# Kernel optimization log

Measured on AMD Instinct MI355X. Metric: run time of the kernel, lower is better.

## Reference

```python
import jax, jax.numpy as jnp
import numpy as np

L2_REG = 0.25

def setup_inputs() -> dict:
    key = jax.random.key(0)
    k0, k1, k2, k3 = jax.random.split(key, 4)
    B, D, A, K = 16384, 128, 8192, 64
    image_embed = jax.random.normal(k0, (B, D), dtype=jnp.float32)
    anc_ind = jax.random.randint(k1, (A,), 0, B, dtype=jnp.int64)
    pos_ind = jax.random.randint(k2, (A,), 0, B, dtype=jnp.int64)
    neg_ind = jax.random.randint(k3, (A, K), 0, B, dtype=jnp.int64)
    return {"image_embed": image_embed, "anc_ind": anc_ind,
            "pos_ind": pos_ind, "neg_ind": neg_ind}

def reference(image_embed, anc_ind, pos_ind, neg_ind):
    # Gather anchor/positive/negative embeddings
    a = image_embed[anc_ind]          # [A, D]
    p = image_embed[pos_ind]          # [A, D]
    n = image_embed[neg_ind]          # [A, K, D]
    # inner[i, k] = a_i . (n_ik - p_i)
    inner = jnp.einsum('ad,akd->ak', a, n - p[:, None, :])  # [A, K]
    # log(1 + sum_k exp(inner)) computed stably via logaddexp(0, logsumexp)
    per_anchor = jnp.logaddexp(jnp.float32(0.0), jax.nn.logsumexp(inner, axis=1))
    npair = jnp.mean(per_anchor)
    # l2 term: mean L2 norm of all batch embeddings, added once per anchor / len -> once
    l2 = L2_REG * jnp.mean(jnp.linalg.norm(image_embed, axis=1))
    return npair + l2
```

## Files before the change

kernel.cpp:

```cpp
#include <hip/hip_runtime.h>
#include <math.h>

#define B_SZ 16384
#define D_DIM 128
#define A_SZ 8192
#define K_SZ 64
#define L2_REG_F 0.25f
#define CONV_BLK 512
#define NBLK 4096
#define NPART (CONV_BLK + NBLK)

typedef float vfloat2 __attribute__((ext_vector_type(2)));

__device__ __forceinline__ float wave_reduce_sum(float v) {
    #pragma unroll
    for (int off = 32; off > 0; off >>= 1)
        v += __shfl_xor(v, off, 64);
    return v;
}

__device__ __forceinline__ float wave_reduce_max(float v) {
    #pragma unroll
    for (int off = 32; off > 0; off >>= 1)
        v = fmaxf(v, __shfl_xor(v, off, 64));
    return v;
}

__device__ __forceinline__ float dot4(float4 a, float4 b) {
    return a.x * b.x + a.y * b.y + a.z * b.z + a.w * b.w;
}

__global__ __launch_bounds__(256) void convert_kernel(const float* __restrict__ embed,
                                                      unsigned short* __restrict__ tab,
                                                      float* __restrict__ partial) {
    __shared__ float red[4];
    const int wave = threadIdx.x >> 6;
    const int lane = threadIdx.x & 63;
    const int gw   = blockIdx.x * 4 + wave;
    float acc = 0.f;
    #pragma unroll
    for (int r = 0; r < B_SZ / (CONV_BLK * 4); ++r) {
        const int row = gw * (B_SZ / (CONV_BLK * 4)) + r;
        const float2* rr = (const float2*)(embed + (size_t)row * D_DIM);
        float2 v = rr[lane];
        acc += sqrtf(wave_reduce_sum(v.x * v.x + v.y * v.y));
        unsigned pk = (unsigned)__builtin_amdgcn_cvt_pk_fp8_f32(v.x, v.y, 0, false);
        tab[(size_t)row * 64 + lane] = (unsigned short)pk;
    }
    if (lane == 0) red[wave] = acc * (L2_REG_F / (float)B_SZ);
    __syncthreads();
    if (threadIdx.x == 0)
        partial[blockIdx.x] = red[0] + red[1] + red[2] + red[3];
}

__global__ __launch_bounds__(256) void fused_kernel(const float* __restrict__ embed,
                                                    const unsigned short* __restrict__ tab,
                                                    const int* __restrict__ anc_ind,
                                                    const int* __restrict__ pos_ind,
                                                    const int* __restrict__ neg_ind,
                                                    float* __restrict__ partial) {
    __shared__ float mw[4], sew[4];
    const int wave = threadIdx.x >> 6;
    const int lane = threadIdx.x & 63;
    const int i    = blockIdx.x * 2 + (wave >> 1);
    const int w    = wave & 1;
    const int g    = lane >> 3;
    const int c    = lane & 7;

    const int4 nb = *(const int4*)(neg_ind + (size_t)i * K_SZ + w * 32 + g * 4);

    const int ai = anc_ind[i];
    const int pi = pos_ind[i];
    const float4* a4 = (const float4*)(embed + (size_t)ai * D_DIM);
    const float4* p4 = (const float4*)(embed + (size_t)pi * D_DIM);
    float4 A0 = a4[c * 4 + 0], A1 = a4[c * 4 + 1];
    float4 A2 = a4[c * 4 + 2], A3 = a4[c * 4 + 3];
    float4 P0 = p4[c * 4 + 0], P1 = p4[c * 4 + 1];
    float4 P2 = p4[c * 4 + 2], P3 = p4[c * 4 + 3];

    uint4 q0 = ((const uint4*)(tab + (size_t)nb.x * 64))[c];
    uint4 q1 = ((const uint4*)(tab + (size_t)nb.y * 64))[c];
    uint4 q2 = ((const uint4*)(tab + (size_t)nb.z * 64))[c];
    uint4 q3 = ((const uint4*)(tab + (size_t)nb.w * 64))[c];

    float app = dot4(A0, P0) + dot4(A1, P1) + dot4(A2, P2) + dot4(A3, P3);
    app += __shfl_xor(app, 1, 64);
    app += __shfl_xor(app, 2, 64);
    app += __shfl_xor(app, 4, 64);

    vfloat2 Av0 = {A0.x, A0.y}, Av1 = {A0.z, A0.w};
    vfloat2 Av2 = {A1.x, A1.y}, Av3 = {A1.z, A1.w};
    vfloat2 Av4 = {A2.x, A2.y}, Av5 = {A2.z, A2.w};
    vfloat2 Av6 = {A3.x, A3.y}, Av7 = {A3.z, A3.w};

    float s[4];
    uint4 qq[4] = {q0, q1, q2, q3};
    #pragma unroll
    for (int p = 0; p < 4; ++p) {
        vfloat2 f0 = __builtin_amdgcn_cvt_pk_f32_fp8(qq[p].x, false);
        vfloat2 f1 = __builtin_amdgcn_cvt_pk_f32_fp8(qq[p].x, true);
        vfloat2 f2 = __builtin_amdgcn_cvt_pk_f32_fp8(qq[p].y, false);
        vfloat2 f3 = __builtin_amdgcn_cvt_pk_f32_fp8(qq[p].y, true);
        vfloat2 f4 = __builtin_amdgcn_cvt_pk_f32_fp8(qq[p].z, false);
        vfloat2 f5 = __builtin_amdgcn_cvt_pk_f32_fp8(qq[p].z, true);
        vfloat2 f6 = __builtin_amdgcn_cvt_pk_f32_fp8(qq[p].w, false);
        vfloat2 f7 = __builtin_amdgcn_cvt_pk_f32_fp8(qq[p].w, true);
        vfloat2 acc = f0 * Av0;
        acc += f1 * Av1;
        acc += f2 * Av2;
        acc += f3 * Av3;
        acc += f4 * Av4;
        acc += f5 * Av5;
        acc += f6 * Av6;
        acc += f7 * Av7;
        s[p] = acc.x + acc.y;
    }

    const bool h4 = (c & 4) != 0;
    float t0 = (h4 ? s[2] : s[0]) + __shfl_xor(h4 ? s[0] : s[2], 4, 64);
    float t1 = (h4 ? s[3] : s[1]) + __shfl_xor(h4 ? s[1] : s[3], 4, 64);
    const bool h2 = (c & 2) != 0;
    float u = (h2 ? t1 : t0) + __shfl_xor(h2 ? t0 : t1, 2, 64);
    u += __shfl_xor(u, 1, 64);
    float inner = u - app;

    float m  = wave_reduce_max(inner);
    float se = 0.5f * wave_reduce_sum(__expf(inner - m));

    if (lane == 0) { mw[wave] = m; sew[wave] = se; }
    __syncthreads();
    if (threadIdx.x == 0) {
        float total = 0.f;
        #pragma unroll
        for (int a = 0; a < 2; ++a) {
            float m0 = mw[2 * a], m1 = mw[2 * a + 1];
            float mm = fmaxf(m0, m1);
            float ss = sew[2 * a] * __expf(m0 - mm) + sew[2 * a + 1] * __expf(m1 - mm);
            float lse = mm + __logf(ss);
            float per = (lse > 0.f) ? lse + log1pf(__expf(-lse)) : log1pf(__expf(lse));
            total += per * (1.0f / (float)A_SZ);
        }
        partial[CONV_BLK + blockIdx.x] = total;
    }
}

__global__ __launch_bounds__(256) void f32_kernel(const float* __restrict__ embed,
                                                  const int* __restrict__ anc_ind,
                                                  const int* __restrict__ pos_ind,
                                                  const int* __restrict__ neg_ind,
                                                  float* __restrict__ partial) {
    __shared__ float mw[4], sew[4], nw[4];
    const int wave = threadIdx.x >> 6;
    const int lane = threadIdx.x & 63;
    const int i    = blockIdx.x * 2 + (wave >> 1);
    const int w    = wave & 1;
    const int g    = lane >> 3;
    const int c    = lane & 7;

    const int4 nb = *(const int4*)(neg_ind + (size_t)i * K_SZ + w * 32 + g * 4);
    const int ai = anc_ind[i];
    const int pi = pos_ind[i];
    const float4* a4 = (const float4*)(embed + (size_t)ai * D_DIM);
    float4 A0 = a4[c], A1 = a4[c + 8], A2 = a4[c + 16], A3 = a4[c + 24];

    const float4* r0 = (const float4*)(embed + (size_t)nb.x * D_DIM);
    const float4* r1 = (const float4*)(embed + (size_t)nb.y * D_DIM);
    const float4* r2 = (const float4*)(embed + (size_t)nb.z * D_DIM);
    const float4* r3 = (const float4*)(embed + (size_t)nb.w * D_DIM);
    float4 q00 = r0[c], q01 = r0[c + 8], q02 = r0[c + 16], q03 = r0[c + 24];
    float4 q10 = r1[c], q11 = r1[c + 8], q12 = r1[c + 16], q13 = r1[c + 24];
    float4 q20 = r2[c], q21 = r2[c + 8], q22 = r2[c + 16], q23 = r2[c + 24];
    float4 q30 = r3[c], q31 = r3[c + 8], q32 = r3[c + 16], q33 = r3[c + 24];

    const float4* p4 = (const float4*)(embed + (size_t)pi * D_DIM);
    float4 P0 = p4[c], P1 = p4[c + 8], P2 = p4[c + 16], P3 = p4[c + 24];
    const int nrow_id = blockIdx.x * 4 + wave;
    float2 nv = ((const float2*)(embed + (size_t)nrow_id * D_DIM))[lane];

    float app = dot4(A0, P0) + dot4(A1, P1) + dot4(A2, P2) + dot4(A3, P3);
    app += __shfl_xor(app, 1, 64);
    app += __shfl_xor(app, 2, 64);
    app += __shfl_xor(app, 4, 64);

    float sq = wave_reduce_sum(nv.x * nv.x + nv.y * nv.y);

    float s0 = dot4(A0, q00) + dot4(A1, q01) + dot4(A2, q02) + dot4(A3, q03);
    float s1 = dot4(A0, q10) + dot4(A1, q11) + dot4(A2, q12) + dot4(A3, q13);
    float s2 = dot4(A0, q20) + dot4(A1, q21) + dot4(A2, q22) + dot4(A3, q23);
    float s3 = dot4(A0, q30) + dot4(A1, q31) + dot4(A2, q32) + dot4(A3, q33);

    const bool h4 = (c & 4) != 0;
    float t0 = (h4 ? s2 : s0) + __shfl_xor(h4 ? s0 : s2, 4, 64);
    float t1 = (h4 ? s3 : s1) + __shfl_xor(h4 ? s1 : s3, 4, 64);
    const bool h2 = (c & 2) != 0;
    float u = (h2 ? t1 : t0) + __shfl_xor(h2 ? t0 : t1, 2, 64);
    u += __shfl_xor(u, 1, 64);
    float inner = u - app;

    float m  = wave_reduce_max(inner);
    float se = 0.5f * wave_reduce_sum(__expf(inner - m));

    if (lane == 0) { mw[wave] = m; sew[wave] = se; nw[wave] = sqrtf(sq); }
    __syncthreads();
    if (threadIdx.x == 0) {
        float total = 0.f;
        #pragma unroll
        for (int a = 0; a < 2; ++a) {
            float m0 = mw[2 * a], m1 = mw[2 * a + 1];
            float mm = fmaxf(m0, m1);
            float ss = sew[2 * a] * __expf(m0 - mm) + sew[2 * a + 1] * __expf(m1 - mm);
            float lse = mm + __logf(ss);
            float per = (lse > 0.f) ? lse + log1pf(__expf(-lse)) : log1pf(__expf(lse));
            total += per * (1.0f / (float)A_SZ);
        }
        total += (nw[0] + nw[1] + nw[2] + nw[3]) * (L2_REG_F / (float)B_SZ);
        partial[blockIdx.x] = total;
    }
}

__global__ __launch_bounds__(256) void finalize_kernel(const float* __restrict__ partial,
                                                       int n, float* __restrict__ out) {
    __shared__ float red[4];
    const int wave = threadIdx.x >> 6;
    const int lane = threadIdx.x & 63;
    float v = 0.f;
    for (int j = threadIdx.x; j < n; j += 256) v += partial[j];
    v = wave_reduce_sum(v);
    if (lane == 0) red[wave] = v;
    __syncthreads();
    if (threadIdx.x == 0)
        out[0] = red[0] + red[1] + red[2] + red[3];
}

extern "C" void kernel_launch(void* const* d_in, const int* in_sizes, int n_in,
                              void* d_out, int out_size, void* d_ws, size_t ws_size,
                              hipStream_t stream) {
    const float* embed = (const float*)d_in[0];
    const int*   anc   = (const int*)d_in[1];
    const int*   pos   = (const int*)d_in[2];
    const int*   neg   = (const int*)d_in[3];
    float* out = (float*)d_out;

    const size_t tab_bytes = (size_t)B_SZ * D_DIM;
    const size_t need = tab_bytes + NPART * sizeof(float);

    if (ws_size >= need) {
        unsigned short* tab = (unsigned short*)d_ws;
        float* partial = (float*)((char*)d_ws + tab_bytes);
        convert_kernel<<<CONV_BLK, 256, 0, stream>>>(embed, tab, partial);
        fused_kernel<<<NBLK, 256, 0, stream>>>(embed, tab, anc, pos, neg, partial);
        finalize_kernel<<<1, 256, 0, stream>>>(partial, NPART, out);
    } else {
        float* partial = (float*)d_ws;
        f32_kernel<<<NBLK, 256, 0, stream>>>(embed, anc, pos, neg, partial);
        finalize_kernel<<<1, 256, 0, stream>>>(partial, NBLK, out);
    }
}
```

Measured before the change: 84.39 us.

## Process one anchor per wave with eight negatives per lane group

The fused kernel now gives each wave a full anchor (64 negatives) instead of splitting an anchor across two waves. Each 8-lane group loads eight negative rows, and the shuffle reduction tree gains a level. This removes the cross-wave shared-memory logsumexp merge, halves the block count and the duplicated anchor/positive loads. The convert kernel also gets more blocks with fewer rows each. The cost is higher register pressure from eight in-flight uint4 loads per lane, which may reduce occupancy.

Measured after the change: 81.55 us. -3.4%, faster.

```diff
diff --git a/kernel.cpp b/kernel.cpp
--- a/kernel.cpp
+++ b/kernel.cpp
@@ -6,8 +6,9 @@
 #define A_SZ 8192
 #define K_SZ 64
 #define L2_REG_F 0.25f
-#define CONV_BLK 512
-#define NBLK 4096
+#define CONV_BLK 2048
+#define NBLK 2048
+#define F32BLK 4096
 #define NPART (CONV_BLK + NBLK)
 
 typedef float vfloat2 __attribute__((ext_vector_type(2)));
@@ -39,8 +40,8 @@
     const int gw   = blockIdx.x * 4 + wave;
     float acc = 0.f;
     #pragma unroll
-    for (int r = 0; r < B_SZ / (CONV_BLK * 4); ++r) {
-        const int row = gw * (B_SZ / (CONV_BLK * 4)) + r;
+    for (int r = 0; r < 2; ++r) {
+        const int row = gw * 2 + r;
         const float2* rr = (const float2*)(embed + (size_t)row * D_DIM);
         float2 v = rr[lane];
         acc += sqrtf(wave_reduce_sum(v.x * v.x + v.y * v.y));
@@ -59,15 +60,15 @@
                                                     const int* __restrict__ pos_ind,
                                                     const int* __restrict__ neg_ind,
                                                     float* __restrict__ partial) {
-    __shared__ float mw[4], sew[4];
-    const int wave = threadIdx.x >> 6;
-    const int lane = threadIdx.x & 63;
-    const int i    = blockIdx.x * 2 + (wave >> 1);
-    const int w    = wave & 1;
+    __shared__ float red[4];
+    const int wave = threadIdx.x >> 6;
+    const int lane = threadIdx.x & 63;
+    const int i    = blockIdx.x * 4 + wave;
     const int g    = lane >> 3;
     const int c    = lane & 7;
 
-    const int4 nb = *(const int4*)(neg_ind + (size_t)i * K_SZ + w * 32 + g * 4);
+    const int4* nbp = (const int4*)(neg_ind + (size_t)i * K_SZ + g * 8);
+    int4 nlo = nbp[0], nhi = nbp[1];
 
     const int ai = anc_ind[i];
     const int pi = pos_ind[i];
@@ -78,10 +79,11 @@
     float4 P0 = p4[c * 4 + 0], P1 = p4[c * 4 + 1];
     float4 P2 = p4[c * 4 + 2], P3 = p4[c * 4 + 3];
 
-    uint4 q0 = ((const uint4*)(tab + (size_t)nb.x * 64))[c];
-    uint4 q1 = ((const uint4*)(tab + (size_t)nb.y * 64))[c];
-    uint4 q2 = ((const uint4*)(tab + (size_t)nb.z * 64))[c];
-    uint4 q3 = ((const uint4*)(tab + (size_t)nb.w * 64))[c];
+    int nidx[8] = {nlo.x, nlo.y, nlo.z, nlo.w, nhi.x, nhi.y, nhi.z, nhi.w};
+    uint4 q[8];
+    #pragma unroll
+    for (int p = 0; p < 8; ++p)
+        q[p] = ((const uint4*)(tab + (size_t)nidx[p] * 64))[c];
 
     float app = dot4(A0, P0) + dot4(A1, P1) + dot4(A2, P2) + dot4(A3, P3);
     app += __shfl_xor(app, 1, 64);
@@ -93,18 +95,17 @@
     vfloat2 Av4 = {A2.x, A2.y}, Av5 = {A2.z, A2.w};
     vfloat2 Av6 = {A3.x, A3.y}, Av7 = {A3.z, A3.w};
 
-    float s[4];
-    uint4 qq[4] = {q0, q1, q2, q3};
-    #pragma unroll
-    for (int p = 0; p < 4; ++p) {
-        vfloat2 f0 = __builtin_amdgcn_cvt_pk_f32_fp8(qq[p].x, false);
-        vfloat2 f1 = __builtin_amdgcn_cvt_pk_f32_fp8(qq[p].x, true);
-        vfloat2 f2 = __builtin_amdgcn_cvt_pk_f32_fp8(qq[p].y, false);
-        vfloat2 f3 = __builtin_amdgcn_cvt_pk_f32_fp8(qq[p].y, true);
-        vfloat2 f4 = __builtin_amdgcn_cvt_pk_f32_fp8(qq[p].z, false);
-        vfloat2 f5 = __builtin_amdgcn_cvt_pk_f32_fp8(qq[p].z, true);
-        vfloat2 f6 = __builtin_amdgcn_cvt_pk_f32_fp8(qq[p].w, false);
-        vfloat2 f7 = __builtin_amdgcn_cvt_pk_f32_fp8(qq[p].w, true);
+    float s[8];
+    #pragma unroll
+    for (int p = 0; p < 8; ++p) {
+        vfloat2 f0 = __builtin_amdgcn_cvt_pk_f32_fp8(q[p].x, false);
+        vfloat2 f1 = __builtin_amdgcn_cvt_pk_f32_fp8(q[p].x, true);
+        vfloat2 f2 = __builtin_amdgcn_cvt_pk_f32_fp8(q[p].y, false);
+        vfloat2 f3 = __builtin_amdgcn_cvt_pk_f32_fp8(q[p].y, true);
+        vfloat2 f4 = __builtin_amdgcn_cvt_pk_f32_fp8(q[p].z, false);
+        vfloat2 f5 = __builtin_amdgcn_cvt_pk_f32_fp8(q[p].z, true);
+        vfloat2 f6 = __builtin_amdgcn_cvt_pk_f32_fp8(q[p].w, false);
+        vfloat2 f7 = __builtin_amdgcn_cvt_pk_f32_fp8(q[p].w, true);
         vfloat2 acc = f0 * Av0;
         acc += f1 * Av1;
         acc += f2 * Av2;
@@ -117,31 +118,27 @@
     }
 
     const bool h4 = (c & 4) != 0;
-    float t0 = (h4 ? s[2] : s[0]) + __shfl_xor(h4 ? s[0] : s[2], 4, 64);
-    float t1 = (h4 ? s[3] : s[1]) + __shfl_xor(h4 ? s[1] : s[3], 4, 64);
+    float t0 = (h4 ? s[4] : s[0]) + __shfl_xor(h4 ? s[0] : s[4], 4, 64);
+    float t1 = (h4 ? s[5] : s[1]) + __shfl_xor(h4 ? s[1] : s[5], 4, 64);
+    float t2 = (h4 ? s[6] : s[2]) + __shfl_xor(h4 ? s[2] : s[6], 4, 64);
+    float t3 = (h4 ? s[7] : s[3]) + __shfl_xor(h4 ? s[3] : s[7], 4, 64);
     const bool h2 = (c & 2) != 0;
-    float u = (h2 ? t1 : t0) + __shfl_xor(h2 ? t0 : t1, 2, 64);
-    u += __shfl_xor(u, 1, 64);
-    float inner = u - app;
+    float u0 = (h2 ? t2 : t0) + __shfl_xor(h2 ? t0 : t2, 2, 64);
+    float u1 = (h2 ? t3 : t1) + __shfl_xor(h2 ? t1 : t3, 2, 64);
+    const bool h1 = (c & 1) != 0;
+    float inner = (h1 ? u1 : u0) + __shfl_xor(h1 ? u0 : u1, 1, 64);
+
+    inner -= app;
 
     float m  = wave_reduce_max(inner);
-    float se = 0.5f * wave_reduce_sum(__expf(inner - m));
-
-    if (lane == 0) { mw[wave] = m; sew[wave] = se; }
-    __syncthreads();
-    if (threadIdx.x == 0) {
-        float total = 0.f;
-        #pragma unroll
-        for (int a = 0; a < 2; ++a) {
-            float m0 = mw[2 * a], m1 = mw[2 * a + 1];
-            float mm = fmaxf(m0, m1);
-            float ss = sew[2 * a] * __expf(m0 - mm) + sew[2 * a + 1] * __expf(m1 - mm);
-            float lse = mm + __logf(ss);
-            float per = (lse > 0.f) ? lse + log1pf(__expf(-lse)) : log1pf(__expf(lse));
-            total += per * (1.0f / (float)A_SZ);
-        }
-        partial[CONV_BLK + blockIdx.x] = total;
-    }
+    float se = wave_reduce_sum(__expf(inner - m));
+    float lse = m + __logf(se);
+    float per = (lse > 0.f) ? lse + log1pf(__expf(-lse)) : log1pf(__expf(lse));
+
+    if (lane == 0) red[wave] = per * (1.0f / (float)A_SZ);
+    __syncthreads();
+    if (threadIdx.x == 0)
+        partial[CONV_BLK + blockIdx.x] = red[0] + red[1] + red[2] + red[3];
 }
 
 __global__ __launch_bounds__(256) void f32_kernel(const float* __restrict__ embed,
@@ -252,7 +249,7 @@
         finalize_kernel<<<1, 256, 0, stream>>>(partial, NPART, out);
     } else {
         float* partial = (float*)d_ws;
-        f32_kernel<<<NBLK, 256, 0, stream>>>(embed, anc, pos, neg, partial);
-        finalize_kernel<<<1, 256, 0, stream>>>(partial, NBLK, out);
-    }
-}
+        f32_kernel<<<F32BLK, 256, 0, stream>>>(embed, anc, pos, neg, partial);
+        finalize_kernel<<<1, 256, 0, stream>>>(partial, F32BLK, out);
+    }
+}
```
